# Performance work log

Hardware: AMD Instinct MI355X
Metric: run time of the kernel (lower is better)

Reference implementation:

```python
import jax, jax.numpy as jnp
import numpy as np

B, C_IN, C_OUT, H, W = 4, 256, 256, 64, 64
KH = KW = 3
STRIDE = 1
PAD = 1
DIL = 1


def setup_inputs() -> dict:
    key = jax.random.key(0)
    k1, k2, k3, k4 = jax.random.split(key, 4)
    x = jax.random.normal(k1, (B, C_IN, H, W), dtype=jnp.float32)
    # torchvision layout: 2*dg*KH*KW channels, (y, x) pair per kernel tap
    offset = jax.random.normal(k2, (B, 2 * KH * KW, H, W), dtype=jnp.float32)
    fan_in = C_IN * KH * KW
    weight = jax.random.normal(k3, (C_OUT, C_IN, KH, KW), dtype=jnp.float32) / np.sqrt(fan_in)
    bias = jax.random.normal(k4, (C_OUT,), dtype=jnp.float32) * 0.01
    return {"x": x, "offset": offset, "weight": weight, "bias": bias}


def _gather_bilinear_corner(x_flat, yi, xi, h, w):
    # x_flat: [B, C, H*W]; yi/xi: [B, KK, Ho, Wo] int32
    valid = ((yi >= 0) & (yi < h) & (xi >= 0) & (xi < w)).astype(x_flat.dtype)
    idx = jnp.clip(yi, 0, h - 1) * w + jnp.clip(xi, 0, w - 1)
    b = idx.shape[0]
    g = jnp.take_along_axis(x_flat, idx.reshape(b, 1, -1), axis=2)
    return g.reshape(b, x_flat.shape[1], *yi.shape[1:]), valid


def deform_conv2d(x, offset, weight, bias):
    b, c, h, w = x.shape
    o = weight.shape[0]
    kk = KH * KW
    ho = (h + 2 * PAD - DIL * (KH - 1) - 1) // STRIDE + 1
    wo = (w + 2 * PAD - DIL * (KW - 1) - 1) // STRIDE + 1

    ky = (jnp.arange(kk, dtype=jnp.float32) // KW) * DIL  # [KK]
    kx = (jnp.arange(kk, dtype=jnp.float32) % KW) * DIL
    hs = jnp.arange(ho, dtype=jnp.float32) * STRIDE - PAD   # [Ho]
    ws = jnp.arange(wo, dtype=jnp.float32) * STRIDE - PAD   # [Wo]

    off = offset.reshape(b, kk, 2, ho, wo)
    py = hs[None, None, :, None] + ky[None, :, None, None] + off[:, :, 0]  # [B,KK,Ho,Wo]
    px = ws[None, None, None, :] + kx[None, :, None, None] + off[:, :, 1]

    y0 = jnp.floor(py)
    x0 = jnp.floor(px)
    wy1 = py - y0  # fractional parts, differentiable w.r.t. offsets
    wx1 = px - x0
    wy0 = 1.0 - wy1
    wx0 = 1.0 - wx1
    y0i = y0.astype(jnp.int32)
    x0i = x0.astype(jnp.int32)

    x_flat = x.reshape(b, c, h * w)
    corners = [
        (y0i,     x0i,     wy0 * wx0),
        (y0i,     x0i + 1, wy0 * wx1),
        (y0i + 1, x0i,     wy1 * wx0),
        (y0i + 1, x0i + 1, wy1 * wx1),
    ]
    sampled = jnp.zeros((b, c, kk, ho, wo), dtype=x.dtype)
    for yi, xi, wgt in corners:
        g, valid = _gather_bilinear_corner(x_flat, yi, xi, h, w)
        sampled = sampled + g * (wgt * valid)[:, None]

    out = jnp.einsum('bckhw,ock->bohw', sampled, weight.reshape(o, c, kk))
    return out + bias[None, :, None, None]


def reference(x, offset, weight, bias):
    return deform_conv2d(x, offset, weight, bias)
```

## Files before the change

kernel.cpp:

```cpp
#include <hip/hip_runtime.h>

typedef __bf16 bf16;
typedef __bf16 bf16x4 __attribute__((ext_vector_type(4)));
typedef __bf16 bf16x8 __attribute__((ext_vector_type(8)));
typedef float  f32x16 __attribute__((ext_vector_type(16)));

#define CIN    256
#define KK     9
#define KDIM   2304
#define KSTEPS 144
#define PXW    32

__device__ __forceinline__ float sread(float f) {
    return __builtin_bit_cast(float,
        __builtin_amdgcn_readfirstlane(__builtin_bit_cast(int, f)));
}
__device__ __forceinline__ int sreadi(int v) {
    return __builtin_amdgcn_readfirstlane(v);
}

__global__ __launch_bounds__(256) void prep_k(const float* __restrict__ x,
                                              const float* __restrict__ w,
                                              bf16* __restrict__ xt,
                                              bf16* __restrict__ wq) {
    int bid = blockIdx.x;
    int tid = threadIdx.x;
    if (bid < 1024) {
        __shared__ bf16 tile[64][72];
        int pt = bid & 63, ct = (bid >> 6) & 3, b = bid >> 8;
        int lane = tid & 63, row = tid >> 6;
        const float* src = x + ((size_t)(b * 256 + ct * 64)) * 4096 + pt * 64;
        #pragma unroll
        for (int cc = row; cc < 64; cc += 4)
            tile[lane][cc] = (bf16)src[(size_t)cc * 4096 + lane];
        __syncthreads();
        bf16* dst = xt + ((size_t)(b * 4096 + pt * 64)) * 256 + ct * 64;
        int p = tid >> 3, j = tid & 7;
        #pragma unroll
        for (int pp = p; pp < 64; pp += 32)
            *reinterpret_cast<bf16x8*>(dst + (size_t)pp * 256 + j * 8) =
                *reinterpret_cast<const bf16x8*>(&tile[pp][j * 8]);
    } else {
        int idx  = (bid - 1024) * 256 + tid;
        int j    = idx & 7;
        int lane = (idx >> 3) & 63;
        int rest = idx >> 9;
        int ks   = rest % KSTEPS;
        int m    = rest / KSTEPS;
        int o    = m * 32 + (lane & 31);
        int k    = ks * 16 + (lane >> 5) * 8 + j;
        int tap  = k >> 8;
        int cc   = k & 255;
        wq[idx] = (bf16)w[(size_t)o * KDIM + cc * KK + tap];
    }
}

__global__ __launch_bounds__(1024, 8) void deform_gemm_k(
    const bf16*  __restrict__ xt,
    const float* __restrict__ off,
    const bf16*  __restrict__ wq,
    const float* __restrict__ bias,
    float*       __restrict__ out) {

    __shared__ bf16 S[2][PXW * 256];

    int tid   = threadIdx.x;
    int wavei = sreadi(tid >> 6);
    int lane  = tid & 63;
    int l32   = lane & 31;
    int half  = lane >> 5;
    int mt    = wavei & 7;
    int kh    = wavei >> 3;

    int bid   = blockIdx.x;
    int pb    = ((bid & 7) << 6) | (bid >> 3);
    int pix0  = pb * PXW;
    int b     = pix0 >> 12;
    int pimgb = pix0 & 4095;
    int obase = b * 73728;
    unsigned base = (unsigned)b * 1048576u + (unsigned)(lane * 4);
    int rot   = ((bid >> 3) & 1) * 4;

    f32x16 acc;
    #pragma unroll
    for (int r = 0; r < 16; ++r) acc[r] = 0.f;

    for (int t = 0; t < KK; ++t) {
        int tap = t + rot; if (tap >= KK) tap -= KK;
        int ty = tap / 3 - 1;
        int tx = tap % 3 - 1;
        bf16* Sw = &S[t & 1][0];

        #pragma unroll
        for (int i = 0; i < 2; ++i) {
            int n    = wavei * 2 + i;
            int pimg = pimgb + n;
            float oy = off[obase + pimg + (2 * tap) * 4096];
            float ox = off[obase + pimg + (2 * tap + 1) * 4096];
            float py = (float)((pimg >> 6) + ty) + oy;
            float px = (float)((pimg & 63) + tx) + ox;
            float fy = floorf(py), fx = floorf(px);
            int   y0 = (int)fy,    x0 = (int)fx;
            float wy1 = py - fy, wx1 = px - fx;
            float wy0 = 1.f - wy1, wx0 = 1.f - wx1;
            wy0 = ((unsigned)y0       < 64u) ? wy0 : 0.f;
            wy1 = ((unsigned)(y0 + 1) < 64u) ? wy1 : 0.f;
            wx0 = ((unsigned)x0       < 64u) ? wx0 : 0.f;
            wx1 = ((unsigned)(x0 + 1) < 64u) ? wx1 : 0.f;
            int yc0 = min(max(y0, 0), 63), yc1 = min(max(y0 + 1, 0), 63);
            int xc0 = min(max(x0, 0), 63), xc1 = min(max(x0 + 1, 0), 63);
            int u0 = sreadi((yc0 * 64 + xc0) * 256);
            int u1 = sreadi((yc0 * 64 + xc1) * 256);
            int u2 = sreadi((yc1 * 64 + xc0) * 256);
            int u3 = sreadi((yc1 * 64 + xc1) * 256);
            float w0 = sread(wy0 * wx0), w1 = sread(wy0 * wx1);
            float w2 = sread(wy1 * wx0), w3 = sread(wy1 * wx1);
            bf16x4 v0 = *reinterpret_cast<const bf16x4*>(xt + base + (unsigned)u0);
            bf16x4 v1 = *reinterpret_cast<const bf16x4*>(xt + base + (unsigned)u1);
            bf16x4 v2 = *reinterpret_cast<const bf16x4*>(xt + base + (unsigned)u2);
            bf16x4 v3 = *reinterpret_cast<const bf16x4*>(xt + base + (unsigned)u3);
            float a0 = w0 * (float)v0[0] + w1 * (float)v1[0]
                     + w2 * (float)v2[0] + w3 * (float)v3[0];
            float a1 = w0 * (float)v0[1] + w1 * (float)v1[1]
                     + w2 * (float)v2[1] + w3 * (float)v3[1];
            float a2 = w0 * (float)v0[2] + w1 * (float)v1[2]
                     + w2 * (float)v2[2] + w3 * (float)v3[2];
            float a3 = w0 * (float)v0[3] + w1 * (float)v1[3]
                     + w2 * (float)v2[3] + w3 * (float)v3[3];
            bf16x4 sv;
            sv[0] = (bf16)a0; sv[1] = (bf16)a1;
            sv[2] = (bf16)a2; sv[3] = (bf16)a3;
            int gs = (lane >> 1) ^ (n & 31);
            *reinterpret_cast<bf16x4*>(Sw + n * 256 + gs * 8 + (lane & 1) * 4) = sv;
        }

        const bf16* ap0 = wq +
            ((size_t)(((mt * KSTEPS) + tap * 16 + kh * 8) * 64 + lane)) * 8;
        bf16x8 a0 = *reinterpret_cast<const bf16x8*>(ap0);
        bf16x8 a1 = *reinterpret_cast<const bf16x8*>(ap0 + 512);
        bf16x8 a2 = *reinterpret_cast<const bf16x8*>(ap0 + 1024);
        bf16x8 a3 = *reinterpret_cast<const bf16x8*>(ap0 + 1536);

        __syncthreads();

        const bf16* Sr = Sw;
        #pragma unroll
        for (int kk2 = 0; kk2 < 8; ++kk2) {
            bf16x8 a;
            if      (kk2 == 0) a = a0;
            else if (kk2 == 1) a = a1;
            else if (kk2 == 2) a = a2;
            else if (kk2 == 3) a = a3;
            else a = *reinterpret_cast<const bf16x8*>(ap0 + (size_t)kk2 * 512);
            int s  = kh * 8 + kk2;
            int g  = s * 2 + half;
            int gs = g ^ l32;
            bf16x8 bf = *reinterpret_cast<const bf16x8*>(Sr + l32 * 256 + gs * 8);
            acc = __builtin_amdgcn_mfma_f32_32x32x16_bf16(a, bf, acc, 0, 0, 0);
        }
    }

    __syncthreads();
    float* Sf = reinterpret_cast<float*>(&S[0][0]);
    if (wavei >= 8) {
        int wb = (wavei - 8) * 64 + lane;
        #pragma unroll
        for (int r = 0; r < 16; ++r)
            Sf[r * 512 + wb] = acc[r];
    }
    __syncthreads();
    if (wavei < 8) {
        int wb   = wavei * 64 + lane;
        int m    = mt * 32;
        int pimg = pimgb + l32;
        float* op = out + ((size_t)(b * 256 + m)) * 4096 + pimg;
        #pragma unroll
        for (int r = 0; r < 16; ++r) {
            int row = (r & 3) + 8 * (r >> 2) + half * 4;
            float v = acc[r] + Sf[r * 512 + wb] + bias[m + row];
            op[(size_t)row * 4096] = v;
        }
    }
}

extern "C" void kernel_launch(void* const* d_in, const int* in_sizes, int n_in,
                              void* d_out, int out_size, void* d_ws, size_t ws_size,
                              hipStream_t stream) {
    const float* x    = (const float*)d_in[0];
    const float* off  = (const float*)d_in[1];
    const float* w    = (const float*)d_in[2];
    const float* bias = (const float*)d_in[3];
    float* out = (float*)d_out;

    bf16* wq = (bf16*)d_ws;
    bf16* xt = (bf16*)((char*)d_ws + (size_t)589824 * 2);

    prep_k<<<3328, 256, 0, stream>>>(x, w, xt, wq);
    deform_gemm_k<<<512, 1024, 0, stream>>>(xt, off, wq, bias, out);
}
```

Measured before the change: 119.7 us.

## Prefetch next tap's bilinear gathers during MFMA and remap lanes per pixel

The bilinear sampling is split into an issue phase and a consume phase. The gathers for the next tap are issued right after the barrier, so their global-load latency overlaps the current tap's MFMA loop. Each half-wave now handles one pixel, so the per-pixel offset math is done once per lane instead of being uniform across the wave. Each lane loads two 8-byte chunks per corner, and bf16-to-fp32 conversion uses bit shifts feeding fmaf. In exchange, register use rises from holding eight uint2 values across the MFMA loop, the early preloading of four weight vectors is dropped, and the scalar readfirstlane addressing is lost.

```diff
diff --git a/kernel.cpp b/kernel.cpp
--- a/kernel.cpp
+++ b/kernel.cpp
@@ -11,10 +11,6 @@
 #define KSTEPS 144
 #define PXW    32
 
-__device__ __forceinline__ float sread(float f) {
-    return __builtin_bit_cast(float,
-        __builtin_amdgcn_readfirstlane(__builtin_bit_cast(int, f)));
-}
 __device__ __forceinline__ int sreadi(int v) {
     return __builtin_amdgcn_readfirstlane(v);
 }
@@ -78,85 +74,99 @@
     int b     = pix0 >> 12;
     int pimgb = pix0 & 4095;
     int obase = b * 73728;
-    unsigned base = (unsigned)b * 1048576u + (unsigned)(lane * 4);
     int rot   = ((bid >> 3) & 1) * 4;
+
+    int n     = wavei * 2 + half;
+    int pimg  = pimgb + n;
+    const char* xb = (const char*)xt + ((size_t)b << 21) + (unsigned)(l32 * 8);
 
     f32x16 acc;
     #pragma unroll
     for (int r = 0; r < 16; ++r) acc[r] = 0.f;
 
+    float wt[4];
+    uint2 g[8];
+
+    auto sample_issue = [&](int tp) {
+        int ty = tp / 3 - 1;
+        int tx = tp % 3 - 1;
+        float oy = off[obase + (2 * tp) * 4096 + pimg];
+        float ox = off[obase + (2 * tp + 1) * 4096 + pimg];
+        float py = (float)((pimg >> 6) + ty) + oy;
+        float px = (float)((pimg & 63) + tx) + ox;
+        float fy = floorf(py), fx = floorf(px);
+        int   y0 = (int)fy,    x0 = (int)fx;
+        float wy1 = py - fy, wx1 = px - fx;
+        float wy0 = 1.f - wy1, wx0 = 1.f - wx1;
+        wy0 = ((unsigned)y0       < 64u) ? wy0 : 0.f;
+        wy1 = ((unsigned)(y0 + 1) < 64u) ? wy1 : 0.f;
+        wx0 = ((unsigned)x0       < 64u) ? wx0 : 0.f;
+        wx1 = ((unsigned)(x0 + 1) < 64u) ? wx1 : 0.f;
+        int yc0 = min(max(y0, 0), 63), yc1 = min(max(y0 + 1, 0), 63);
+        int xc0 = min(max(x0, 0), 63), xc1 = min(max(x0 + 1, 0), 63);
+        unsigned u0 = (unsigned)(yc0 * 64 + xc0) * 512u;
+        unsigned u1 = (unsigned)(yc0 * 64 + xc1) * 512u;
+        unsigned u2 = (unsigned)(yc1 * 64 + xc0) * 512u;
+        unsigned u3 = (unsigned)(yc1 * 64 + xc1) * 512u;
+        wt[0] = wy0 * wx0; wt[1] = wy0 * wx1;
+        wt[2] = wy1 * wx0; wt[3] = wy1 * wx1;
+        g[0] = *reinterpret_cast<const uint2*>(xb + u0);
+        g[1] = *reinterpret_cast<const uint2*>(xb + u0 + 256);
+        g[2] = *reinterpret_cast<const uint2*>(xb + u1);
+        g[3] = *reinterpret_cast<const uint2*>(xb + u1 + 256);
+        g[4] = *reinterpret_cast<const uint2*>(xb + u2);
+        g[5] = *reinterpret_cast<const uint2*>(xb + u2 + 256);
+        g[6] = *reinterpret_cast<const uint2*>(xb + u3);
+        g[7] = *reinterpret_cast<const uint2*>(xb + u3 + 256);
+    };
+
+    int tapc = rot;
+    sample_issue(tapc);
+
     for (int t = 0; t < KK; ++t) {
-        int tap = t + rot; if (tap >= KK) tap -= KK;
-        int ty = tap / 3 - 1;
-        int tx = tap % 3 - 1;
         bf16* Sw = &S[t & 1][0];
 
         #pragma unroll
-        for (int i = 0; i < 2; ++i) {
-            int n    = wavei * 2 + i;
-            int pimg = pimgb + n;
-            float oy = off[obase + pimg + (2 * tap) * 4096];
-            float ox = off[obase + pimg + (2 * tap + 1) * 4096];
-            float py = (float)((pimg >> 6) + ty) + oy;
-            float px = (float)((pimg & 63) + tx) + ox;
-            float fy = floorf(py), fx = floorf(px);
-            int   y0 = (int)fy,    x0 = (int)fx;
-            float wy1 = py - fy, wx1 = px - fx;
-            float wy0 = 1.f - wy1, wx0 = 1.f - wx1;
-            wy0 = ((unsigned)y0       < 64u) ? wy0 : 0.f;
-            wy1 = ((unsigned)(y0 + 1) < 64u) ? wy1 : 0.f;
-            wx0 = ((unsigned)x0       < 64u) ? wx0 : 0.f;
-            wx1 = ((unsigned)(x0 + 1) < 64u) ? wx1 : 0.f;
-            int yc0 = min(max(y0, 0), 63), yc1 = min(max(y0 + 1, 0), 63);
-            int xc0 = min(max(x0, 0), 63), xc1 = min(max(x0 + 1, 0), 63);
-            int u0 = sreadi((yc0 * 64 + xc0) * 256);
-            int u1 = sreadi((yc0 * 64 + xc1) * 256);
-            int u2 = sreadi((yc1 * 64 + xc0) * 256);
-            int u3 = sreadi((yc1 * 64 + xc1) * 256);
-            float w0 = sread(wy0 * wx0), w1 = sread(wy0 * wx1);
-            float w2 = sread(wy1 * wx0), w3 = sread(wy1 * wx1);
-            bf16x4 v0 = *reinterpret_cast<const bf16x4*>(xt + base + (unsigned)u0);
-            bf16x4 v1 = *reinterpret_cast<const bf16x4*>(xt + base + (unsigned)u1);
-            bf16x4 v2 = *reinterpret_cast<const bf16x4*>(xt + base + (unsigned)u2);
-            bf16x4 v3 = *reinterpret_cast<const bf16x4*>(xt + base + (unsigned)u3);
-            float a0 = w0 * (float)v0[0] + w1 * (float)v1[0]
-                     + w2 * (float)v2[0] + w3 * (float)v3[0];
-            float a1 = w0 * (float)v0[1] + w1 * (float)v1[1]
-                     + w2 * (float)v2[1] + w3 * (float)v3[1];
-            float a2 = w0 * (float)v0[2] + w1 * (float)v1[2]
-                     + w2 * (float)v2[2] + w3 * (float)v3[2];
-            float a3 = w0 * (float)v0[3] + w1 * (float)v1[3]
-                     + w2 * (float)v2[3] + w3 * (float)v3[3];
+        for (int p = 0; p < 2; ++p) {
+            float a0 = 0.f, a1 = 0.f, a2 = 0.f, a3 = 0.f;
+            #pragma unroll
+            for (int c = 0; c < 4; ++c) {
+                uint2 v = g[c * 2 + p];
+                float f0 = __builtin_bit_cast(float, v.x << 16);
+                float f1 = __builtin_bit_cast(float, v.x & 0xffff0000u);
+                float f2 = __builtin_bit_cast(float, v.y << 16);
+                float f3 = __builtin_bit_cast(float, v.y & 0xffff0000u);
+                a0 = fmaf(wt[c], f0, a0);
+                a1 = fmaf(wt[c], f1, a1);
+                a2 = fmaf(wt[c], f2, a2);
+                a3 = fmaf(wt[c], f3, a3);
+            }
             bf16x4 sv;
             sv[0] = (bf16)a0; sv[1] = (bf16)a1;
             sv[2] = (bf16)a2; sv[3] = (bf16)a3;
-            int gs = (lane >> 1) ^ (n & 31);
-            *reinterpret_cast<bf16x4*>(Sw + n * 256 + gs * 8 + (lane & 1) * 4) = sv;
-        }
-
+            int gsw = ((p * 16) + (l32 >> 1)) ^ n;
+            *reinterpret_cast<bf16x4*>(Sw + n * 256 + gsw * 8 + (l32 & 1) * 4) = sv;
+        }
+
+        __syncthreads();
+
+        int tapg = tapc;
+        if (t < KK - 1) {
+            int tn = tapc + 1; if (tn >= KK) tn = 0;
+            tapc = tn;
+            sample_issue(tn);
+        }
+
+        const bf16* Sr  = Sw;
         const bf16* ap0 = wq +
-            ((size_t)(((mt * KSTEPS) + tap * 16 + kh * 8) * 64 + lane)) * 8;
-        bf16x8 a0 = *reinterpret_cast<const bf16x8*>(ap0);
-        bf16x8 a1 = *reinterpret_cast<const bf16x8*>(ap0 + 512);
-        bf16x8 a2 = *reinterpret_cast<const bf16x8*>(ap0 + 1024);
-        bf16x8 a3 = *reinterpret_cast<const bf16x8*>(ap0 + 1536);
-
-        __syncthreads();
-
-        const bf16* Sr = Sw;
+            ((size_t)(((mt * KSTEPS) + tapg * 16 + kh * 8) * 64 + lane)) * 8;
         #pragma unroll
         for (int kk2 = 0; kk2 < 8; ++kk2) {
-            bf16x8 a;
-            if      (kk2 == 0) a = a0;
-            else if (kk2 == 1) a = a1;
-            else if (kk2 == 2) a = a2;
-            else if (kk2 == 3) a = a3;
-            else a = *reinterpret_cast<const bf16x8*>(ap0 + (size_t)kk2 * 512);
-            int s  = kh * 8 + kk2;
-            int g  = s * 2 + half;
-            int gs = g ^ l32;
-            bf16x8 bf = *reinterpret_cast<const bf16x8*>(Sr + l32 * 256 + gs * 8);
-            acc = __builtin_amdgcn_mfma_f32_32x32x16_bf16(a, bf, acc, 0, 0, 0);
+            bf16x8 a = *reinterpret_cast<const bf16x8*>(ap0 + (size_t)kk2 * 512);
+            int gg  = (kh * 8 + kk2) * 2 + half;
+            int gsr = gg ^ l32;
+            bf16x8 bv = *reinterpret_cast<const bf16x8*>(Sr + l32 * 256 + gsr * 8);
+            acc = __builtin_amdgcn_mfma_f32_32x32x16_bf16(a, bv, acc, 0, 0, 0);
         }
     }
 
@@ -172,8 +182,8 @@
     if (wavei < 8) {
         int wb   = wavei * 64 + lane;
         int m    = mt * 32;
-        int pimg = pimgb + l32;
-        float* op = out + ((size_t)(b * 256 + m)) * 4096 + pimg;
+        int pimo = pimgb + l32;
+        float* op = out + ((size_t)(b * 256 + m)) * 4096 + pimo;
         #pragma unroll
         for (int r = 0; r < 16; ++r) {
             int row = (r & 3) + 8 * (r >> 2) + half * 4;
```

After: 144.7 us. 1.21x slower.
